# Optimization experiments

Measured on AMD Instinct MI355X. Metric: run time of the kernel, lower is better.

The kernel has to match this reference:

```python
import jax, jax.numpy as jnp
import numpy as np

H, W, D = 160, 160, 16
VOXEL_SIZE = 0.4
VOL_MIN = np.array([-32.0, -32.0, -1.0], dtype=np.float32)
SCALE_MULTIPLIER = 3.0
N_GAUSS = 8192
CHUNK = 64


def setup_inputs() -> dict:
    key = jax.random.key(0)
    k1, k2, k3, k4, k5 = jax.random.split(key, 5)
    vol_min = jnp.asarray(VOL_MIN)
    vol_ext = jnp.array([64.0, 64.0, 6.4], dtype=jnp.float32)
    means3d = jax.random.uniform(k1, (N_GAUSS, 3), jnp.float32) * vol_ext + vol_min
    opacities = jax.random.uniform(k2, (N_GAUSS, 1), jnp.float32)
    # per-axis std devs: 0.2..0.8 m so 3-sigma footprint spans a handful of voxels
    scales = 0.2 + 0.6 * jax.random.uniform(k3, (N_GAUSS, 3), jnp.float32)
    rotations = jax.random.normal(k4, (N_GAUSS, 4), jnp.float32)
    features = jax.random.normal(k5, (N_GAUSS, 32), jnp.float32)
    return {"means3d": means3d, "opacities": opacities, "scales": scales,
            "rotations": rotations, "features": features}


def quat_to_rotmat(q):
    # q: [N,4] wxyz, normalized
    w, x, y, z = q[:, 0], q[:, 1], q[:, 2], q[:, 3]
    R = jnp.stack([
        jnp.stack([1 - 2 * (y * y + z * z), 2 * (x * y - w * z), 2 * (x * z + w * y)], -1),
        jnp.stack([2 * (x * y + w * z), 1 - 2 * (x * x + z * z), 2 * (y * z - w * x)], -1),
        jnp.stack([2 * (x * z - w * y), 2 * (y * z + w * x), 1 - 2 * (x * x + y * y)], -1),
    ], axis=-2)  # [N,3,3]
    return R


def _grid_coords():
    ii, jj, kk = jnp.meshgrid(jnp.arange(H), jnp.arange(W), jnp.arange(D), indexing="ij")
    idx = jnp.stack([ii, jj, kk], axis=-1).astype(jnp.float32)
    return (idx + 0.5) * VOXEL_SIZE + jnp.asarray(VOL_MIN)  # [H,W,D,3] voxel centers


def reference(means3d, opacities, scales, rotations, features):
    x = _grid_coords().reshape(-1, 3)  # [V,3]
    q = rotations / jnp.linalg.norm(rotations, axis=-1, keepdims=True)
    R = quat_to_rotmat(q)
    # covariance = R diag(s^2) R^T
    cov = jnp.einsum("nij,nj,nkj->nik", R, scales * scales, R)
    cov_inv = jnp.linalg.inv(cov)
    sigma = jnp.sqrt(jnp.diagonal(cov, axis1=1, axis2=2))  # [N,3]
    opac = opacities[:, 0]  # [N]
    n = means3d.shape[0]
    nchunks = n // CHUNK

    def chunked(a):
        return a.reshape(nchunks, CHUNK, *a.shape[1:])

    def step(acc, c):
        mu, op, sg, ci, ft = c
        diff = x[:, None, :] - mu[None, :, :]  # [V,CHUNK,3]
        maha = jnp.einsum("vci,cij,vcj->vc", diff, ci, diff)
        # local aggregation cutoff: within scale_multiplier * sigma box around mean
        mask = jnp.all(jnp.abs(diff) <= SCALE_MULTIPLIER * sg[None, :, :], axis=-1)
        w = op[None, :] * jnp.exp(-0.5 * maha) * mask  # [V,CHUNK]
        return acc + w @ ft, None

    acc0 = jnp.zeros((x.shape[0], features.shape[-1]), jnp.float32)
    xs = (chunked(means3d), chunked(opac), chunked(sigma), chunked(cov_inv), chunked(features))
    acc, _ = jax.lax.scan(step, acc0, xs)
    return acc.reshape(H, W, D, features.shape[-1])
```

## Files before the change

kernel.cpp:

```cpp
#include <hip/hip_runtime.h>

#define HH 160
#define WW 160
#define DD 16
#define NG 8192
#define VOXEL 0.4f

#define TTX 20
#define TTY 20
#define TTZ 4
#define NTILES (TTX * TTY * TTZ)
#define CAP 256


__global__ __launch_bounds__(256) void gv_precompute_bin(
    const float* __restrict__ means, const float* __restrict__ opac,
    const float* __restrict__ scales, const float* __restrict__ rots,
    float4* __restrict__ pack, int* __restrict__ tileCnt,
    int* __restrict__ tileList) {
  int g = blockIdx.x * 256 + threadIdx.x;
  if (g >= NG) return;
  float qw = rots[g * 4 + 0], qx = rots[g * 4 + 1];
  float qy = rots[g * 4 + 2], qz = rots[g * 4 + 3];
  float inv = rsqrtf(qw * qw + qx * qx + qy * qy + qz * qz);
  qw *= inv; qx *= inv; qy *= inv; qz *= inv;
  float R[3][3];
  R[0][0] = 1.f - 2.f * (qy * qy + qz * qz);
  R[0][1] = 2.f * (qx * qy - qw * qz);
  R[0][2] = 2.f * (qx * qz + qw * qy);
  R[1][0] = 2.f * (qx * qy + qw * qz);
  R[1][1] = 1.f - 2.f * (qx * qx + qz * qz);
  R[1][2] = 2.f * (qy * qz - qw * qx);
  R[2][0] = 2.f * (qx * qz - qw * qy);
  R[2][1] = 2.f * (qy * qz + qw * qx);
  R[2][2] = 1.f - 2.f * (qx * qx + qy * qy);
  float sx = scales[g * 3 + 0], sy = scales[g * 3 + 1], sz = scales[g * 3 + 2];
  float s2[3] = {sx * sx, sy * sy, sz * sz};
  float is2[3] = {1.f / s2[0], 1.f / s2[1], 1.f / s2[2]};
  float cov00 = 0.f, cov11 = 0.f, cov22 = 0.f;
  float ci00 = 0.f, ci01 = 0.f, ci02 = 0.f, ci11 = 0.f, ci12 = 0.f, ci22 = 0.f;
#pragma unroll
  for (int c = 0; c < 3; c++) {
    cov00 += R[0][c] * R[0][c] * s2[c];
    cov11 += R[1][c] * R[1][c] * s2[c];
    cov22 += R[2][c] * R[2][c] * s2[c];
    ci00 += R[0][c] * R[0][c] * is2[c];
    ci01 += R[0][c] * R[1][c] * is2[c];
    ci02 += R[0][c] * R[2][c] * is2[c];
    ci11 += R[1][c] * R[1][c] * is2[c];
    ci12 += R[1][c] * R[2][c] * is2[c];
    ci22 += R[2][c] * R[2][c] * is2[c];
  }
  float mx = means[g * 3 + 0], my = means[g * 3 + 1], mz = means[g * 3 + 2];
  float bx = 3.f * sqrtf(cov00), by = 3.f * sqrtf(cov11), bz = 3.f * sqrtf(cov22);
  float4* p = pack + (size_t)g * 4;
  p[0] = make_float4(mx, my, mz, opac[g]);
  p[1] = make_float4(bx, by, bz, ci00);
  p[2] = make_float4(ci01, ci02, ci11, ci12);
  p[3] = make_float4(ci22, 0.f, 0.f, 0.f);

  const float eps = 1e-4f;
  int i0 = (int)ceilf((mx - bx + 32.f) * 2.5f - 0.5f - eps);
  int i1 = (int)floorf((mx + bx + 32.f) * 2.5f - 0.5f + eps);
  int j0 = (int)ceilf((my - by + 32.f) * 2.5f - 0.5f - eps);
  int j1 = (int)floorf((my + by + 32.f) * 2.5f - 0.5f + eps);
  int k0 = (int)ceilf((mz - bz + 1.f) * 2.5f - 0.5f - eps);
  int k1 = (int)floorf((mz + bz + 1.f) * 2.5f - 0.5f + eps);
  i0 = max(i0, 0); i1 = min(i1, HH - 1);
  j0 = max(j0, 0); j1 = min(j1, WW - 1);
  k0 = max(k0, 0); k1 = min(k1, DD - 1);
  if (i0 > i1 || j0 > j1 || k0 > k1) return;
  int ti0 = i0 >> 3, ti1 = i1 >> 3;
  int tj0 = j0 >> 3, tj1 = j1 >> 3;
  int tk0 = k0 >> 2, tk1 = k1 >> 2;
  for (int ti = ti0; ti <= ti1; ti++)
    for (int tj = tj0; tj <= tj1; tj++)
      for (int tk = tk0; tk <= tk1; tk++) {
        int t = (ti * TTY + tj) * TTZ + tk;
        int pos = atomicAdd(&tileCnt[t], 1);
        if (pos < CAP) tileList[t * CAP + pos] = g;
      }
}

#define CHUNK_SZ 64

__global__ __launch_bounds__(256) void gv_voxelize(
    const float4* __restrict__ pack, const float4* __restrict__ feats,
    const int* __restrict__ tileCnt, const int* __restrict__ tileList,
    float4* __restrict__ out) {
  __shared__ float4 s_pack[CHUNK_SZ * 4];
  __shared__ float4 s_feat[CHUNK_SZ * 8];

  int tid = threadIdx.x;
  int dk = tid & 3, dj = (tid >> 2) & 7, di = tid >> 5;
  int tk = blockIdx.x, tj = blockIdx.y, ti = blockIdx.z;
  int i = ti * 8 + di, j = tj * 8 + dj, k = tk * 4 + dk;

  float px = (i + 0.5f) * VOXEL - 32.f;
  float py = (j + 0.5f) * VOXEL - 32.f;
  float pz = (k + 0.5f) * VOXEL - 1.f;

  int t = (ti * TTY + tj) * TTZ + tk;
  int cnt = tileCnt[t];
  cnt = min(cnt, CAP);
  const int* lst = tileList + t * CAP;

  float4 acc[8];
#pragma unroll
  for (int f = 0; f < 8; f++) acc[f] = make_float4(0.f, 0.f, 0.f, 0.f);

  for (int base = 0; base < cnt; base += CHUNK_SZ) {
    int M = min(CHUNK_SZ, cnt - base);
    __syncthreads();
    {
      int m = tid >> 2, w = tid & 3;
      if (m < M) {
        int gg = lst[base + m];
        s_pack[m * 4 + w] = pack[(size_t)gg * 4 + w];
      }
    }
#pragma unroll
    for (int r = 0; r < 2; r++) {
      int idx = tid + 256 * r;
      int m = idx >> 3, f = idx & 7;
      if (m < M) {
        int gg = lst[base + m];
        s_feat[m * 8 + f] = feats[(size_t)gg * 8 + f];
      }
    }
    __syncthreads();

    for (int n = 0; n < M; n++) {
      float4 pa = s_pack[n * 4 + 0];
      float4 pb = s_pack[n * 4 + 1];
      float dx = px - pa.x, dy = py - pa.y, dz = pz - pa.z;
      bool in = (fabsf(dx) <= pb.x) & (fabsf(dy) <= pb.y) & (fabsf(dz) <= pb.z);
      if (__any(in)) {
        float4 pc = s_pack[n * 4 + 2];
        float4 pd = s_pack[n * 4 + 3];
        float maha = pb.w * dx * dx + pc.z * dy * dy + pd.x * dz * dz +
                     2.f * (pc.x * dx * dy + pc.y * dx * dz + pc.w * dy * dz);
        float w = in ? pa.w * __expf(-0.5f * maha) : 0.f;
#pragma unroll
        for (int f = 0; f < 8; f++) {
          float4 fv = s_feat[n * 8 + f];
          acc[f].x += w * fv.x;
          acc[f].y += w * fv.y;
          acc[f].z += w * fv.z;
          acc[f].w += w * fv.w;
        }
      }
    }
  }

  size_t v = ((size_t)i * WW + j) * DD + k;
  float4* o = out + v * 8;
#pragma unroll
  for (int f = 0; f < 8; f++) o[f] = acc[f];
}

extern "C" void kernel_launch(void* const* d_in, const int* in_sizes, int n_in,
                              void* d_out, int out_size, void* d_ws, size_t ws_size,
                              hipStream_t stream) {
  const float* means  = (const float*)d_in[0];
  const float* opac   = (const float*)d_in[1];
  const float* scales = (const float*)d_in[2];
  const float* rots   = (const float*)d_in[3];
  const float4* feats = (const float4*)d_in[4];

  char* ws = (char*)d_ws;
  float4* pack   = (float4*)ws;
  int* tileCnt   = (int*)(ws + 512 * 1024);
  int* tileList  = (int*)(ws + 520 * 1024);

  hipMemsetAsync(tileCnt, 0, NTILES * sizeof(int), stream);
  gv_precompute_bin<<<32, 256, 0, stream>>>(means, opac, scales, rots,
                                            pack, tileCnt, tileList);
  dim3 grid(TTZ, TTY, TTX);
  gv_voxelize<<<grid, 256, 0, stream>>>(pack, feats, tileCnt, tileList,
                                        (float4*)d_out);
}
```

Before: 128.1 us.

## Drop shared-memory staging in voxelize; read gaussian data directly from global

The voxelize kernel no longer stages each chunk of gaussian parameters and features into shared memory behind two barriers. Each thread now reads the tile list, packed parameters and features straight from global memory, relying on wavefront-uniform addresses and the caches for broadcast. The binning kernel is relaunched with 64-thread blocks to spread its work across more CUs. This removes barrier stalls and the upfront loading of features for gaussians that end up culled, but makes each thread issue redundant global loads and adds load latency inside the inner loop.

```diff
diff --git a/kernel.cpp b/kernel.cpp
--- a/kernel.cpp
+++ b/kernel.cpp
@@ -13,12 +13,12 @@
 #define CAP 256
 
 
-__global__ __launch_bounds__(256) void gv_precompute_bin(
+__global__ __launch_bounds__(64) void gv_precompute_bin(
     const float* __restrict__ means, const float* __restrict__ opac,
     const float* __restrict__ scales, const float* __restrict__ rots,
     float4* __restrict__ pack, int* __restrict__ tileCnt,
     int* __restrict__ tileList) {
-  int g = blockIdx.x * 256 + threadIdx.x;
+  int g = blockIdx.x * 64 + threadIdx.x;
   if (g >= NG) return;
   float qw = rots[g * 4 + 0], qx = rots[g * 4 + 1];
   float qy = rots[g * 4 + 2], qz = rots[g * 4 + 3];
@@ -82,15 +82,10 @@
       }
 }
 
-#define CHUNK_SZ 64
-
 __global__ __launch_bounds__(256) void gv_voxelize(
     const float4* __restrict__ pack, const float4* __restrict__ feats,
     const int* __restrict__ tileCnt, const int* __restrict__ tileList,
     float4* __restrict__ out) {
-  __shared__ float4 s_pack[CHUNK_SZ * 4];
-  __shared__ float4 s_feat[CHUNK_SZ * 8];
-
   int tid = threadIdx.x;
   int dk = tid & 3, dj = (tid >> 2) & 7, di = tid >> 5;
   int tk = blockIdx.x, tj = blockIdx.y, ti = blockIdx.z;
@@ -101,54 +96,35 @@
   float pz = (k + 0.5f) * VOXEL - 1.f;
 
   int t = (ti * TTY + tj) * TTZ + tk;
-  int cnt = tileCnt[t];
-  cnt = min(cnt, CAP);
+  int cnt = min(tileCnt[t], CAP);
   const int* lst = tileList + t * CAP;
 
   float4 acc[8];
 #pragma unroll
   for (int f = 0; f < 8; f++) acc[f] = make_float4(0.f, 0.f, 0.f, 0.f);
 
-  for (int base = 0; base < cnt; base += CHUNK_SZ) {
-    int M = min(CHUNK_SZ, cnt - base);
-    __syncthreads();
-    {
-      int m = tid >> 2, w = tid & 3;
-      if (m < M) {
-        int gg = lst[base + m];
-        s_pack[m * 4 + w] = pack[(size_t)gg * 4 + w];
-      }
-    }
+#pragma unroll 2
+  for (int n = 0; n < cnt; n++) {
+    int gg = lst[n];
+    const float4* p = pack + (size_t)gg * 4;
+    float4 pa = p[0];
+    float4 pb = p[1];
+    float dx = px - pa.x, dy = py - pa.y, dz = pz - pa.z;
+    bool in = (fabsf(dx) <= pb.x) & (fabsf(dy) <= pb.y) & (fabsf(dz) <= pb.z);
+    if (__any(in)) {
+      float4 pc = p[2];
+      float4 pd = p[3];
+      float maha = pb.w * dx * dx + pc.z * dy * dy + pd.x * dz * dz +
+                   2.f * (pc.x * dx * dy + pc.y * dx * dz + pc.w * dy * dz);
+      float w = in ? pa.w * __expf(-0.5f * maha) : 0.f;
+      const float4* ft = feats + (size_t)gg * 8;
 #pragma unroll
-    for (int r = 0; r < 2; r++) {
-      int idx = tid + 256 * r;
-      int m = idx >> 3, f = idx & 7;
-      if (m < M) {
-        int gg = lst[base + m];
-        s_feat[m * 8 + f] = feats[(size_t)gg * 8 + f];
-      }
-    }
-    __syncthreads();
-
-    for (int n = 0; n < M; n++) {
-      float4 pa = s_pack[n * 4 + 0];
-      float4 pb = s_pack[n * 4 + 1];
-      float dx = px - pa.x, dy = py - pa.y, dz = pz - pa.z;
-      bool in = (fabsf(dx) <= pb.x) & (fabsf(dy) <= pb.y) & (fabsf(dz) <= pb.z);
-      if (__any(in)) {
-        float4 pc = s_pack[n * 4 + 2];
-        float4 pd = s_pack[n * 4 + 3];
-        float maha = pb.w * dx * dx + pc.z * dy * dy + pd.x * dz * dz +
-                     2.f * (pc.x * dx * dy + pc.y * dx * dz + pc.w * dy * dz);
-        float w = in ? pa.w * __expf(-0.5f * maha) : 0.f;
-#pragma unroll
-        for (int f = 0; f < 8; f++) {
-          float4 fv = s_feat[n * 8 + f];
-          acc[f].x += w * fv.x;
-          acc[f].y += w * fv.y;
-          acc[f].z += w * fv.z;
-          acc[f].w += w * fv.w;
-        }
+      for (int f = 0; f < 8; f++) {
+        float4 fv = ft[f];
+        acc[f].x += w * fv.x;
+        acc[f].y += w * fv.y;
+        acc[f].z += w * fv.z;
+        acc[f].w += w * fv.w;
       }
     }
   }
@@ -174,8 +150,8 @@
   int* tileList  = (int*)(ws + 520 * 1024);
 
   hipMemsetAsync(tileCnt, 0, NTILES * sizeof(int), stream);
-  gv_precompute_bin<<<32, 256, 0, stream>>>(means, opac, scales, rots,
-                                            pack, tileCnt, tileList);
+  gv_precompute_bin<<<NG / 64, 64, 0, stream>>>(means, opac, scales, rots,
+                                                pack, tileCnt, tileList);
   dim3 grid(TTZ, TTY, TTX);
   gv_voxelize<<<grid, 256, 0, stream>>>(pack, feats, tileCnt, tileList,
                                         (float4*)d_out);
```

After: 138.2 us. +7.8%, slower.
